# Performance work log

Hardware: AMD Instinct MI355X
Metric: run time of the kernel (lower is better)

## Reference

```python
import jax, jax.numpy as jnp
import numpy as np
from jax import lax

GAMMA = 0.99
TAU = 0.95
B = 4194304  # batchsz (flat trajectory length)


def setup_inputs() -> dict:
    key = jax.random.key(0)
    k_r, k_v, k_m = jax.random.split(key, 3)
    r = jax.random.normal(k_r, (B,), dtype=jnp.float32)
    v = jax.random.normal(k_v, (B,), dtype=jnp.float32)
    mask = jax.random.randint(k_m, (B,), 0, 2, dtype=jnp.int32)  # 0 = episode end
    return {"r": r, "v": v, "mask": mask}


def reference(r, v, mask):
    """GAE advantage + V-target via a reverse linear-recurrence scan.

    v_target[t] = r[t] + gamma * v_target[t+1] * mask[t]
    delta[t]    = r[t] + gamma * v[t+1]        * mask[t] - v[t]
    A_sa[t]     = delta[t] + gamma * tau * A_sa[t+1] * mask[t]
    A_sa normalized to zero mean / unit (unbiased) std, as in torch .std().
    """
    m = mask.astype(r.dtype)

    def step(carry, x):
        prev_vt, prev_v, prev_A = carry
        r_t, v_t, m_t = x
        vt = r_t + GAMMA * prev_vt * m_t
        delta = r_t + GAMMA * prev_v * m_t - v_t
        A = delta + GAMMA * TAU * prev_A * m_t
        return (vt, v_t, A), (vt, A)

    zero = jnp.float32(0.0)
    _, (v_target, A_sa) = lax.scan(step, (zero, zero, zero), (r, v, m), reverse=True)
    A_sa = (A_sa - A_sa.mean()) / jnp.std(A_sa, ddof=1)
    return A_sa, v_target
```

## Files before the change

kernel.cpp:

```cpp
#include <hip/hip_runtime.h>
#include <math.h>

#define BTOT 4194304
#define TPB  256
#define EPT  16
#define CS   (TPB * EPT)
#define NCH  (BTOT / CS)
#define CPT  (NCH / TPB)


__constant__ const float kG  = 0.99f;
__constant__ const float kGT = 0.99f * 0.95f;

__device__ __forceinline__ float wave_red(float x) {
#pragma unroll
    for (int o = 32; o > 0; o >>= 1) x += __shfl_down(x, o);
    return x;
}

__global__ __launch_bounds__(TPB) void k1_summarize(
    const float* __restrict__ r, const float* __restrict__ v,
    const int* __restrict__ mk, float* __restrict__ ws) {
    const int c = blockIdx.x;
    const int j = threadIdx.x;
    const int base = c * CS + j * EPT;

    float rr[EPT], vv[EPT + 1], dd[EPT];
    int mm[EPT];
    const float4* r4 = (const float4*)(r + base);
    const float4* v4 = (const float4*)(v + base);
    const int4*   m4 = (const int4*)(mk + base);
#pragma unroll
    for (int k = 0; k < EPT / 4; ++k) {
        float4 a = r4[k];
        rr[4*k] = a.x; rr[4*k+1] = a.y; rr[4*k+2] = a.z; rr[4*k+3] = a.w;
        float4 b = v4[k];
        vv[4*k] = b.x; vv[4*k+1] = b.y; vv[4*k+2] = b.z; vv[4*k+3] = b.w;
        int4 m = m4[k];
        mm[4*k] = m.x; mm[4*k+1] = m.y; mm[4*k+2] = m.z; mm[4*k+3] = m.w;
    }
    vv[EPT] = (base + EPT < BTOT) ? v[base + EPT] : 0.0f;

#pragma unroll
    for (int k = 0; k < EPT; ++k) {
        float m = (float)mm[k];
        dd[k] = rr[k] + kG * m * vv[k + 1] - vv[k];
    }

    float pv = 1.0f, sv = 0.0f, pa = 1.0f, sa = 0.0f;
#pragma unroll
    for (int k = EPT - 1; k >= 0; --k) {
        float m = (float)mm[k];
        float av = kG * m, aa = kGT * m;
        sv = rr[k] + av * sv;
        sa = dd[k] + aa * sa;
        pv *= av; pa *= aa;
    }

    __shared__ float lpv[TPB], lsv[TPB], lpa[TPB], lsa[TPB];
    lpv[j] = pv; lsv[j] = sv; lpa[j] = pa; lsa[j] = sa;
    __syncthreads();
#pragma unroll
    for (int d = 1; d < TPB; d <<= 1) {
        float cpv = lpv[j], csv = lsv[j], cpa = lpa[j], csa = lsa[j];
        bool has = (j + d) < TPB;
        float qpv = 1.0f, qsv = 0.0f, qpa = 1.0f, qsa = 0.0f;
        if (has) { qpv = lpv[j+d]; qsv = lsv[j+d]; qpa = lpa[j+d]; qsa = lsa[j+d]; }
        __syncthreads();
        if (has) {
            lpv[j] = cpv * qpv; lsv[j] = csv + cpv * qsv;
            lpa[j] = cpa * qpa; lsa[j] = csa + cpa * qsa;
        }
        __syncthreads();
    }
    float CinA = (j + 1 < TPB) ? lsa[j + 1] : 0.0f;
    float QrA  = (j + 1 < TPB) ? lpa[j + 1] : 1.0f;
    float chPv = lpv[0], chSv = lsv[0], chPa = lpa[0], chSa = lsa[0];

    float x = CinA, ql = 1.0f;
    float s0 = 0, s1 = 0, s2 = 0, s3 = 0, s4 = 0;
#pragma unroll
    for (int k = EPT - 1; k >= 0; --k) {
        float m = (float)mm[k];
        float aa = kGT * m;
        x = dd[k] + aa * x;
        ql *= aa;
        float q = ql * QrA;
        s0 += x; s1 += q; s2 += x * x; s3 += x * q; s4 += q * q;
    }
    s0 = wave_red(s0); s1 = wave_red(s1); s2 = wave_red(s2);
    s3 = wave_red(s3); s4 = wave_red(s4);
    __shared__ float rb[4][5];
    int wid = j >> 6, ln = j & 63;
    if (ln == 0) { rb[wid][0]=s0; rb[wid][1]=s1; rb[wid][2]=s2; rb[wid][3]=s3; rb[wid][4]=s4; }
    __syncthreads();
    if (j == 0) {
        float t0=0,t1=0,t2=0,t3=0,t4=0;
        for (int w = 0; w < 4; ++w) { t0+=rb[w][0]; t1+=rb[w][1]; t2+=rb[w][2]; t3+=rb[w][3]; t4+=rb[w][4]; }
        ws[0*NCH+c] = chPv; ws[1*NCH+c] = chSv; ws[2*NCH+c] = chPa; ws[3*NCH+c] = chSa;
        ws[4*NCH+c] = t0;   ws[5*NCH+c] = t1;   ws[6*NCH+c] = t2;
        ws[7*NCH+c] = t3;   ws[8*NCH+c] = t4;
    }
}

__global__ __launch_bounds__(TPB) void k2_scan_chunks(float* __restrict__ ws) {
    const int j = threadIdx.x;
    const float* Pv  = ws + 0*NCH; const float* Sv  = ws + 1*NCH;
    const float* Pa  = ws + 2*NCH; const float* Sa  = ws + 3*NCH;
    const float* sL  = ws + 4*NCH; const float* sq  = ws + 5*NCH;
    const float* sL2 = ws + 6*NCH; const float* sLq = ws + 7*NCH;
    const float* sq2 = ws + 8*NCH;
    float* Cv_ = ws + 9*NCH; float* Ca_ = ws + 10*NCH;

    float pv = 1.0f, sv = 0.0f, pa = 1.0f, sa = 0.0f;
#pragma unroll
    for (int i = j*CPT + CPT - 1; i >= j*CPT; --i) {
        sv = Sv[i] + Pv[i] * sv; pv = Pv[i] * pv;
        sa = Sa[i] + Pa[i] * sa; pa = Pa[i] * pa;
    }
    __shared__ float lpv[TPB], lsv[TPB], lpa[TPB], lsa[TPB];
    lpv[j] = pv; lsv[j] = sv; lpa[j] = pa; lsa[j] = sa;
    __syncthreads();
#pragma unroll
    for (int d = 1; d < TPB; d <<= 1) {
        float cpv = lpv[j], csv = lsv[j], cpa = lpa[j], csa = lsa[j];
        bool has = (j + d) < TPB;
        float qpv = 1.0f, qsv = 0.0f, qpa = 1.0f, qsa = 0.0f;
        if (has) { qpv = lpv[j+d]; qsv = lsv[j+d]; qpa = lpa[j+d]; qsa = lsa[j+d]; }
        __syncthreads();
        if (has) {
            lpv[j] = cpv * qpv; lsv[j] = csv + cpv * qsv;
            lpa[j] = cpa * qpa; lsa[j] = csa + cpa * qsa;
        }
        __syncthreads();
    }
    float Cv = (j + 1 < TPB) ? lsv[j + 1] : 0.0f;
    float Ca = (j + 1 < TPB) ? lsa[j + 1] : 0.0f;

    double dS = 0.0, dS2 = 0.0;
#pragma unroll
    for (int i = j*CPT + CPT - 1; i >= j*CPT; --i) {
        Cv_[i] = Cv; Ca_[i] = Ca;
        dS  += (double)(sL[i]  + Ca * sq[i]);
        dS2 += (double)(sL2[i] + 2.0f * Ca * sLq[i] + Ca * Ca * sq2[i]);
        Cv = Sv[i] + Pv[i] * Cv;
        Ca = Sa[i] + Pa[i] * Ca;
    }
#pragma unroll
    for (int o = 32; o > 0; o >>= 1) { dS += __shfl_down(dS, o); dS2 += __shfl_down(dS2, o); }
    __shared__ double r1[4], r2[4];
    int wid = j >> 6, ln = j & 63;
    if (ln == 0) { r1[wid] = dS; r2[wid] = dS2; }
    __syncthreads();
    if (j == 0) {
        double S  = r1[0] + r1[1] + r1[2] + r1[3];
        double S2 = r2[0] + r2[1] + r2[2] + r2[3];
        double n = (double)BTOT;
        double mean = S / n;
        double var = (S2 - S * mean) / (n - 1.0);
        ws[11*NCH]     = (float)mean;
        ws[11*NCH + 1] = (float)(1.0 / sqrt(var));
    }
}

__global__ __launch_bounds__(TPB) void k3_finalize(
    const float* __restrict__ r, const float* __restrict__ v,
    const int* __restrict__ mk, const float* __restrict__ ws,
    float* __restrict__ outA, float* __restrict__ outV) {
    const int c = blockIdx.x;
    const int j = threadIdx.x;
    const int base = c * CS + j * EPT;

    float rr[EPT], vv[EPT + 1], dd[EPT];
    int mm[EPT];
    const float4* r4 = (const float4*)(r + base);
    const float4* v4 = (const float4*)(v + base);
    const int4*   m4 = (const int4*)(mk + base);
#pragma unroll
    for (int k = 0; k < EPT / 4; ++k) {
        float4 a = r4[k];
        rr[4*k] = a.x; rr[4*k+1] = a.y; rr[4*k+2] = a.z; rr[4*k+3] = a.w;
        float4 b = v4[k];
        vv[4*k] = b.x; vv[4*k+1] = b.y; vv[4*k+2] = b.z; vv[4*k+3] = b.w;
        int4 m = m4[k];
        mm[4*k] = m.x; mm[4*k+1] = m.y; mm[4*k+2] = m.z; mm[4*k+3] = m.w;
    }
    vv[EPT] = (base + EPT < BTOT) ? v[base + EPT] : 0.0f;
#pragma unroll
    for (int k = 0; k < EPT; ++k) {
        float m = (float)mm[k];
        dd[k] = rr[k] + kG * m * vv[k + 1] - vv[k];
    }

    float pv = 1.0f, sv = 0.0f, pa = 1.0f, sa = 0.0f;
#pragma unroll
    for (int k = EPT - 1; k >= 0; --k) {
        float m = (float)mm[k];
        float av = kG * m, aa = kGT * m;
        sv = rr[k] + av * sv;
        sa = dd[k] + aa * sa;
        pv *= av; pa *= aa;
    }
    __shared__ float lpv[TPB], lsv[TPB], lpa[TPB], lsa[TPB];
    lpv[j] = pv; lsv[j] = sv; lpa[j] = pa; lsa[j] = sa;
    __syncthreads();
#pragma unroll
    for (int d = 1; d < TPB; d <<= 1) {
        float cpv = lpv[j], csv = lsv[j], cpa = lpa[j], csa = lsa[j];
        bool has = (j + d) < TPB;
        float qpv = 1.0f, qsv = 0.0f, qpa = 1.0f, qsa = 0.0f;
        if (has) { qpv = lpv[j+d]; qsv = lsv[j+d]; qpa = lpa[j+d]; qsa = lsa[j+d]; }
        __syncthreads();
        if (has) {
            lpv[j] = cpv * qpv; lsv[j] = csv + cpv * qsv;
            lpa[j] = cpa * qpa; lsa[j] = csa + cpa * qsa;
        }
        __syncthreads();
    }
    float CinV = (j + 1 < TPB) ? lsv[j + 1] : 0.0f;
    float QrV  = (j + 1 < TPB) ? lpv[j + 1] : 1.0f;
    float CinA = (j + 1 < TPB) ? lsa[j + 1] : 0.0f;
    float QrA  = (j + 1 < TPB) ? lpa[j + 1] : 1.0f;

    float Ccv = ws[9*NCH + c];
    float Cca = ws[10*NCH + c];
    float mean = ws[11*NCH];
    float inv  = ws[11*NCH + 1];

    float xv = CinV + QrV * Ccv;
    float xa = CinA + QrA * Cca;
    float oA[EPT], oV[EPT];
#pragma unroll
    for (int k = EPT - 1; k >= 0; --k) {
        float m = (float)mm[k];
        xv = rr[k] + kG  * m * xv;
        xa = dd[k] + kGT * m * xa;
        oV[k] = xv;
        oA[k] = (xa - mean) * inv;
    }
    float4* a4 = (float4*)(outA + base);
    float4* w4 = (float4*)(outV + base);
#pragma unroll
    for (int k = 0; k < EPT / 4; ++k) {
        a4[k] = make_float4(oA[4*k], oA[4*k+1], oA[4*k+2], oA[4*k+3]);
        w4[k] = make_float4(oV[4*k], oV[4*k+1], oV[4*k+2], oV[4*k+3]);
    }
}

extern "C" void kernel_launch(void* const* d_in, const int* in_sizes, int n_in,
                              void* d_out, int out_size, void* d_ws, size_t ws_size,
                              hipStream_t stream) {
    const float* r  = (const float*)d_in[0];
    const float* v  = (const float*)d_in[1];
    const int*   mk = (const int*)d_in[2];
    float* out = (float*)d_out;
    float* ws  = (float*)d_ws;

    hipLaunchKernelGGL(k1_summarize, dim3(NCH), dim3(TPB), 0, stream, r, v, mk, ws);
    hipLaunchKernelGGL(k2_scan_chunks, dim3(1), dim3(TPB), 0, stream, ws);
    hipLaunchKernelGGL(k3_finalize, dim3(NCH), dim3(TPB), 0, stream,
                       r, v, mk, ws, out, out + BTOT);
}
```

Baseline: 116.9 us.

## Fold single-block chunk scan into finalize kernel, recomputed redundantly per block

Removes the single-block middle kernel that scanned the 1024 chunk summaries and computed mean/std. Each finalize block now reads all chunk summaries itself, runs the cross-chunk scan and double-precision statistics reduction redundantly, and takes its own carry-in and normalization constants from shared memory. This drops one launch and a serialized one-block stage, at the cost of every block re-reading about 36 KB of workspace and doing extra scan work before its main pass.

After: 115.3 us. About the same (-1.4%).

```diff
diff --git a/kernel.cpp b/kernel.cpp
--- a/kernel.cpp
+++ b/kernel.cpp
@@ -12,13 +12,39 @@
 __constant__ const float kG  = 0.99f;
 __constant__ const float kGT = 0.99f * 0.95f;
 
-__device__ __forceinline__ float wave_red(float x) {
+__device__ __forceinline__ float wave_redf(float x) {
 #pragma unroll
     for (int o = 32; o > 0; o >>= 1) x += __shfl_down(x, o);
     return x;
 }
-
-__global__ __launch_bounds__(TPB) void k1_summarize(
+__device__ __forceinline__ double wave_redd(double x) {
+#pragma unroll
+    for (int o = 32; o > 0; o >>= 1) x += __shfl_down(x, o);
+    return x;
+}
+
+__device__ __forceinline__ void block_suffix_scan(
+    float pv, float sv, float pa, float sa,
+    float* lpv, float* lsv, float* lpa, float* lsa, int j)
+{
+    lpv[j] = pv; lsv[j] = sv; lpa[j] = pa; lsa[j] = sa;
+    __syncthreads();
+#pragma unroll
+    for (int d = 1; d < TPB; d <<= 1) {
+        float cpv = lpv[j], csv = lsv[j], cpa = lpa[j], csa = lsa[j];
+        bool has = (j + d) < TPB;
+        float qpv = 1.0f, qsv = 0.0f, qpa = 1.0f, qsa = 0.0f;
+        if (has) { qpv = lpv[j+d]; qsv = lsv[j+d]; qpa = lpa[j+d]; qsa = lsa[j+d]; }
+        __syncthreads();
+        if (has) {
+            lpv[j] = cpv * qpv; lsv[j] = csv + cpv * qsv;
+            lpa[j] = cpa * qpa; lsa[j] = csa + cpa * qsa;
+        }
+        __syncthreads();
+    }
+}
+
+__global__ __launch_bounds__(TPB) void ppo_k1_summarize(
     const float* __restrict__ r, const float* __restrict__ v,
     const int* __restrict__ mk, float* __restrict__ ws) {
     const int c = blockIdx.x;
@@ -58,21 +84,8 @@
     }
 
     __shared__ float lpv[TPB], lsv[TPB], lpa[TPB], lsa[TPB];
-    lpv[j] = pv; lsv[j] = sv; lpa[j] = pa; lsa[j] = sa;
-    __syncthreads();
-#pragma unroll
-    for (int d = 1; d < TPB; d <<= 1) {
-        float cpv = lpv[j], csv = lsv[j], cpa = lpa[j], csa = lsa[j];
-        bool has = (j + d) < TPB;
-        float qpv = 1.0f, qsv = 0.0f, qpa = 1.0f, qsa = 0.0f;
-        if (has) { qpv = lpv[j+d]; qsv = lsv[j+d]; qpa = lpa[j+d]; qsa = lsa[j+d]; }
-        __syncthreads();
-        if (has) {
-            lpv[j] = cpv * qpv; lsv[j] = csv + cpv * qsv;
-            lpa[j] = cpa * qpa; lsa[j] = csa + cpa * qsa;
-        }
-        __syncthreads();
-    }
+    block_suffix_scan(pv, sv, pa, sa, lpv, lsv, lpa, lsa, j);
+
     float CinA = (j + 1 < TPB) ? lsa[j + 1] : 0.0f;
     float QrA  = (j + 1 < TPB) ? lpa[j + 1] : 1.0f;
     float chPv = lpv[0], chSv = lsv[0], chPa = lpa[0], chSa = lsa[0];
@@ -88,8 +101,8 @@
         float q = ql * QrA;
         s0 += x; s1 += q; s2 += x * x; s3 += x * q; s4 += q * q;
     }
-    s0 = wave_red(s0); s1 = wave_red(s1); s2 = wave_red(s2);
-    s3 = wave_red(s3); s4 = wave_red(s4);
+    s0 = wave_redf(s0); s1 = wave_redf(s1); s2 = wave_redf(s2);
+    s3 = wave_redf(s3); s4 = wave_redf(s4);
     __shared__ float rb[4][5];
     int wid = j >> 6, ln = j & 63;
     if (ln == 0) { rb[wid][0]=s0; rb[wid][1]=s1; rb[wid][2]=s2; rb[wid][3]=s3; rb[wid][4]=s4; }
@@ -103,73 +116,74 @@
     }
 }
 
-__global__ __launch_bounds__(TPB) void k2_scan_chunks(float* __restrict__ ws) {
-    const int j = threadIdx.x;
-    const float* Pv  = ws + 0*NCH; const float* Sv  = ws + 1*NCH;
-    const float* Pa  = ws + 2*NCH; const float* Sa  = ws + 3*NCH;
-    const float* sL  = ws + 4*NCH; const float* sq  = ws + 5*NCH;
-    const float* sL2 = ws + 6*NCH; const float* sLq = ws + 7*NCH;
-    const float* sq2 = ws + 8*NCH;
-    float* Cv_ = ws + 9*NCH; float* Ca_ = ws + 10*NCH;
-
-    float pv = 1.0f, sv = 0.0f, pa = 1.0f, sa = 0.0f;
-#pragma unroll
-    for (int i = j*CPT + CPT - 1; i >= j*CPT; --i) {
-        sv = Sv[i] + Pv[i] * sv; pv = Pv[i] * pv;
-        sa = Sa[i] + Pa[i] * sa; pa = Pa[i] * pa;
-    }
-    __shared__ float lpv[TPB], lsv[TPB], lpa[TPB], lsa[TPB];
-    lpv[j] = pv; lsv[j] = sv; lpa[j] = pa; lsa[j] = sa;
-    __syncthreads();
-#pragma unroll
-    for (int d = 1; d < TPB; d <<= 1) {
-        float cpv = lpv[j], csv = lsv[j], cpa = lpa[j], csa = lsa[j];
-        bool has = (j + d) < TPB;
-        float qpv = 1.0f, qsv = 0.0f, qpa = 1.0f, qsa = 0.0f;
-        if (has) { qpv = lpv[j+d]; qsv = lsv[j+d]; qpa = lpa[j+d]; qsa = lsa[j+d]; }
-        __syncthreads();
-        if (has) {
-            lpv[j] = cpv * qpv; lsv[j] = csv + cpv * qsv;
-            lpa[j] = cpa * qpa; lsa[j] = csa + cpa * qsa;
-        }
-        __syncthreads();
-    }
-    float Cv = (j + 1 < TPB) ? lsv[j + 1] : 0.0f;
-    float Ca = (j + 1 < TPB) ? lsa[j + 1] : 0.0f;
-
-    double dS = 0.0, dS2 = 0.0;
-#pragma unroll
-    for (int i = j*CPT + CPT - 1; i >= j*CPT; --i) {
-        Cv_[i] = Cv; Ca_[i] = Ca;
-        dS  += (double)(sL[i]  + Ca * sq[i]);
-        dS2 += (double)(sL2[i] + 2.0f * Ca * sLq[i] + Ca * Ca * sq2[i]);
-        Cv = Sv[i] + Pv[i] * Cv;
-        Ca = Sa[i] + Pa[i] * Ca;
-    }
-#pragma unroll
-    for (int o = 32; o > 0; o >>= 1) { dS += __shfl_down(dS, o); dS2 += __shfl_down(dS2, o); }
-    __shared__ double r1[4], r2[4];
-    int wid = j >> 6, ln = j & 63;
-    if (ln == 0) { r1[wid] = dS; r2[wid] = dS2; }
-    __syncthreads();
-    if (j == 0) {
-        double S  = r1[0] + r1[1] + r1[2] + r1[3];
-        double S2 = r2[0] + r2[1] + r2[2] + r2[3];
-        double n = (double)BTOT;
-        double mean = S / n;
-        double var = (S2 - S * mean) / (n - 1.0);
-        ws[11*NCH]     = (float)mean;
-        ws[11*NCH + 1] = (float)(1.0 / sqrt(var));
-    }
-}
-
-__global__ __launch_bounds__(TPB) void k3_finalize(
+__global__ __launch_bounds__(TPB) void ppo_k2_finalize(
     const float* __restrict__ r, const float* __restrict__ v,
     const int* __restrict__ mk, const float* __restrict__ ws,
-    float* __restrict__ outA, float* __restrict__ outV) {
+    float* __restrict__ outA, float* __restrict__ outV)
+{
     const int c = blockIdx.x;
     const int j = threadIdx.x;
     const int base = c * CS + j * EPT;
+
+    __shared__ float lpv[TPB], lsv[TPB], lpa[TPB], lsa[TPB];
+    __shared__ double rd[4][2];
+    __shared__ float bcast[4];
+
+    {
+        float cpv[CPT], csv[CPT], cpa[CPT], csa[CPT];
+        {
+            float4 t;
+            t = *(const float4*)(ws + 0*NCH + 4*j); cpv[0]=t.x; cpv[1]=t.y; cpv[2]=t.z; cpv[3]=t.w;
+            t = *(const float4*)(ws + 1*NCH + 4*j); csv[0]=t.x; csv[1]=t.y; csv[2]=t.z; csv[3]=t.w;
+            t = *(const float4*)(ws + 2*NCH + 4*j); cpa[0]=t.x; cpa[1]=t.y; cpa[2]=t.z; cpa[3]=t.w;
+            t = *(const float4*)(ws + 3*NCH + 4*j); csa[0]=t.x; csa[1]=t.y; csa[2]=t.z; csa[3]=t.w;
+        }
+        float gpv = 1.0f, gsv = 0.0f, gpa = 1.0f, gsa = 0.0f;
+#pragma unroll
+        for (int i = CPT - 1; i >= 0; --i) {
+            gsv = csv[i] + cpv[i] * gsv; gpv = cpv[i] * gpv;
+            gsa = csa[i] + cpa[i] * gsa; gpa = cpa[i] * gpa;
+        }
+
+        block_suffix_scan(gpv, gsv, gpa, gsa, lpv, lsv, lpa, lsa, j);
+
+        float Cv = (j + 1 < TPB) ? lsv[j + 1] : 0.0f;
+        float Ca = (j + 1 < TPB) ? lsa[j + 1] : 0.0f;
+
+        float sLv[CPT], sqv[CPT], sL2v[CPT], sLqv[CPT], sq2v[CPT];
+        {
+            float4 t;
+            t = *(const float4*)(ws + 4*NCH + 4*j); sLv[0]=t.x;  sLv[1]=t.y;  sLv[2]=t.z;  sLv[3]=t.w;
+            t = *(const float4*)(ws + 5*NCH + 4*j); sqv[0]=t.x;  sqv[1]=t.y;  sqv[2]=t.z;  sqv[3]=t.w;
+            t = *(const float4*)(ws + 6*NCH + 4*j); sL2v[0]=t.x; sL2v[1]=t.y; sL2v[2]=t.z; sL2v[3]=t.w;
+            t = *(const float4*)(ws + 7*NCH + 4*j); sLqv[0]=t.x; sLqv[1]=t.y; sLqv[2]=t.z; sLqv[3]=t.w;
+            t = *(const float4*)(ws + 8*NCH + 4*j); sq2v[0]=t.x; sq2v[1]=t.y; sq2v[2]=t.z; sq2v[3]=t.w;
+        }
+        double dS = 0.0, dS2 = 0.0;
+#pragma unroll
+        for (int i = CPT - 1; i >= 0; --i) {
+            int g = 4*j + i;
+            if (g == c) { bcast[0] = Cv; bcast[1] = Ca; }
+            dS  += (double)(sLv[i]  + Ca * sqv[i]);
+            dS2 += (double)(sL2v[i] + 2.0f * Ca * sLqv[i] + Ca * Ca * sq2v[i]);
+            Cv = csv[i] + cpv[i] * Cv;
+            Ca = csa[i] + cpa[i] * Ca;
+        }
+        dS = wave_redd(dS); dS2 = wave_redd(dS2);
+        int wid = j >> 6, ln = j & 63;
+        if (ln == 0) { rd[wid][0] = dS; rd[wid][1] = dS2; }
+        __syncthreads();
+        if (j == 0) {
+            double S  = rd[0][0] + rd[1][0] + rd[2][0] + rd[3][0];
+            double S2 = rd[0][1] + rd[1][1] + rd[2][1] + rd[3][1];
+            double n = (double)BTOT;
+            double mean = S / n;
+            double var = (S2 - S * mean) / (n - 1.0);
+            bcast[2] = (float)mean;
+            bcast[3] = (float)(1.0 / sqrt(var));
+        }
+        __syncthreads();
+    }
 
     float rr[EPT], vv[EPT + 1], dd[EPT];
     int mm[EPT];
@@ -201,31 +215,17 @@
         sa = dd[k] + aa * sa;
         pv *= av; pa *= aa;
     }
-    __shared__ float lpv[TPB], lsv[TPB], lpa[TPB], lsa[TPB];
-    lpv[j] = pv; lsv[j] = sv; lpa[j] = pa; lsa[j] = sa;
-    __syncthreads();
-#pragma unroll
-    for (int d = 1; d < TPB; d <<= 1) {
-        float cpv = lpv[j], csv = lsv[j], cpa = lpa[j], csa = lsa[j];
-        bool has = (j + d) < TPB;
-        float qpv = 1.0f, qsv = 0.0f, qpa = 1.0f, qsa = 0.0f;
-        if (has) { qpv = lpv[j+d]; qsv = lsv[j+d]; qpa = lpa[j+d]; qsa = lsa[j+d]; }
-        __syncthreads();
-        if (has) {
-            lpv[j] = cpv * qpv; lsv[j] = csv + cpv * qsv;
-            lpa[j] = cpa * qpa; lsa[j] = csa + cpa * qsa;
-        }
-        __syncthreads();
-    }
+    block_suffix_scan(pv, sv, pa, sa, lpv, lsv, lpa, lsa, j);
+
     float CinV = (j + 1 < TPB) ? lsv[j + 1] : 0.0f;
     float QrV  = (j + 1 < TPB) ? lpv[j + 1] : 1.0f;
     float CinA = (j + 1 < TPB) ? lsa[j + 1] : 0.0f;
     float QrA  = (j + 1 < TPB) ? lpa[j + 1] : 1.0f;
 
-    float Ccv = ws[9*NCH + c];
-    float Cca = ws[10*NCH + c];
-    float mean = ws[11*NCH];
-    float inv  = ws[11*NCH + 1];
+    const float Ccv  = bcast[0];
+    const float Cca  = bcast[1];
+    const float mean = bcast[2];
+    const float inv  = bcast[3];
 
     float xv = CinV + QrV * Ccv;
     float xa = CinA + QrA * Cca;
@@ -253,11 +253,12 @@
     const float* r  = (const float*)d_in[0];
     const float* v  = (const float*)d_in[1];
     const int*   mk = (const int*)d_in[2];
-    float* out = (float*)d_out;
-    float* ws  = (float*)d_ws;
-
-    hipLaunchKernelGGL(k1_summarize, dim3(NCH), dim3(TPB), 0, stream, r, v, mk, ws);
-    hipLaunchKernelGGL(k2_scan_chunks, dim3(1), dim3(TPB), 0, stream, ws);
-    hipLaunchKernelGGL(k3_finalize, dim3(NCH), dim3(TPB), 0, stream,
-                       r, v, mk, ws, out, out + BTOT);
-}
+    float* outA = (float*)d_out;
+    float* outV = outA + BTOT;
+    float* ws   = (float*)d_ws;
+
+    hipLaunchKernelGGL(ppo_k1_summarize, dim3(NCH), dim3(TPB), 0, stream,
+                       r, v, mk, ws);
+    hipLaunchKernelGGL(ppo_k2_finalize, dim3(NCH), dim3(TPB), 0, stream,
+                       r, v, mk, ws, outA, outV);
+}
```
